# Kernel tuning notes

Measured on AMD Instinct MI355X. Metric: run time of the kernel, lower is better.

## Reference

```python
import jax, jax.numpy as jnp
import numpy as np

N_NODES = 50000
N_EDGES = 800000
IN_FEATS, N_HIDDEN, OUT_FEATS = 512, 512, 256


def setup_inputs() -> dict:
    key = jax.random.key(0)
    ks = jax.random.split(key, 10)
    features = jax.random.normal(ks[0], (N_NODES, IN_FEATS), dtype=jnp.float32)
    src = jax.random.randint(ks[1], (N_EDGES,), 0, N_NODES, dtype=jnp.int64)
    dst = jax.random.randint(ks[2], (N_EDGES,), 0, N_NODES, dtype=jnp.int64)
    def glorot(k, fan_in, fan_out):
        s = jnp.sqrt(6.0 / (fan_in + fan_out)).astype(jnp.float32)
        return jax.random.uniform(k, (fan_in, fan_out), jnp.float32, -s, s)
    W0 = glorot(ks[3], IN_FEATS, N_HIDDEN)
    b0 = jnp.zeros((N_HIDDEN,), jnp.float32)
    W1 = glorot(ks[4], N_HIDDEN, N_HIDDEN)
    b1 = jnp.zeros((N_HIDDEN,), jnp.float32)
    W2 = glorot(ks[5], N_HIDDEN, OUT_FEATS)
    b2 = jnp.zeros((OUT_FEATS,), jnp.float32)
    return {"features": features, "src": src, "dst": dst,
            "W0": W0, "b0": b0, "W1": W1, "b1": b1, "W2": W2, "b2": b2}


def _graph_conv(x, W, b, src, dst, out_norm, in_norm, activation):
    # DGL GraphConv, norm='both': D_out^{-1/2} A^T D_in^{-1/2}? -> per-node scale,
    # gather on src, segment-sum on dst, scale, linear, bias, activation.
    h = x @ W                               # [N, out] dense GEMM (weight applied first)
    h = h * out_norm[:, None]               # src-side degree norm
    msgs = h[src]                           # [E, out] gather
    agg = jax.ops.segment_sum(msgs, dst, num_segments=x.shape[0])  # [N, out]
    agg = agg * in_norm[:, None] + b
    return activation(agg) if activation is not None else agg


def reference(features, src, dst, W0, b0, W1, b1, W2, b2):
    n = features.shape[0]
    ones = jnp.ones((src.shape[0],), jnp.float32)
    out_deg = jnp.clip(jax.ops.segment_sum(ones, src, num_segments=n), 1.0)
    in_deg = jnp.clip(jax.ops.segment_sum(ones, dst, num_segments=n), 1.0)
    out_norm = jax.lax.rsqrt(out_deg)
    in_norm = jax.lax.rsqrt(in_deg)
    # eval mode: dropout between layers is identity
    h = _graph_conv(features, W0, b0, src, dst, out_norm, in_norm, jax.nn.relu)
    h = _graph_conv(h, W1, b1, src, dst, out_norm, in_norm, jax.nn.relu)
    h = _graph_conv(h, W2, b2, src, dst, out_norm, in_norm, None)
    return h
```

## Files before the change

### kernel.cpp

```cpp
#include <hip/hip_runtime.h>

#define N_NODES 50000
#define N_EDGES 800000

typedef __attribute__((ext_vector_type(8))) _Float16 half8;
typedef __attribute__((ext_vector_type(4))) float f32x4;
typedef __attribute__((ext_vector_type(8))) unsigned short ushort8;

static __device__ __forceinline__ unsigned short f2h(float f) {
    _Float16 h = (_Float16)f;
    return __builtin_bit_cast(unsigned short, h);
}
static __device__ __forceinline__ float h2f(unsigned short u) {
    return (float)__builtin_bit_cast(_Float16, u);
}

static __device__ __forceinline__ void async16(unsigned short* lds, const unsigned short* g) {
    __builtin_amdgcn_global_load_lds(
        (const __attribute__((address_space(1))) void*)g,
        (__attribute__((address_space(3))) void*)lds, 16, 0, 0);
}

__global__ void hist_kernel(const int* __restrict__ src, const int* __restrict__ dst,
                            int* __restrict__ outc, int* __restrict__ inc) {
    int i = blockIdx.x * blockDim.x + threadIdx.x;
    if (i < N_EDGES) {
        atomicAdd(&outc[src[i]], 1);
        atomicAdd(&inc[dst[i]], 1);
    }
}

__global__ void norm_kernel(const int* __restrict__ outc, const int* __restrict__ inc,
                            float* __restrict__ outn, float* __restrict__ inn) {
    int i = blockIdx.x * blockDim.x + threadIdx.x;
    if (i < N_NODES) {
        outn[i] = rsqrtf(fmaxf((float)outc[i], 1.0f));
        inn[i]  = rsqrtf(fmaxf((float)inc[i], 1.0f));
    }
}

__global__ __launch_bounds__(256) void scan1(const int* __restrict__ cnt,
                                             int* __restrict__ row_start,
                                             int* __restrict__ bsum, int n) {
    __shared__ int t[256];
    int tid = threadIdx.x;
    int i = blockIdx.x * 256 + tid;
    int v = (i < n) ? cnt[i] : 0;
    t[tid] = v;
    __syncthreads();
#pragma unroll
    for (int off = 1; off < 256; off <<= 1) {
        int x = (tid >= off) ? t[tid - off] : 0;
        __syncthreads();
        t[tid] += x;
        __syncthreads();
    }
    if (i < n) row_start[i] = t[tid] - v;
    if (tid == 255) bsum[blockIdx.x] = t[255];
}

__global__ __launch_bounds__(256) void scan2(int* __restrict__ bsum,
                                             int* __restrict__ boff,
                                             int* __restrict__ row_start, int nb) {
    __shared__ int t[256];
    int tid = threadIdx.x;
    int v = (tid < nb) ? bsum[tid] : 0;
    t[tid] = v;
    __syncthreads();
#pragma unroll
    for (int off = 1; off < 256; off <<= 1) {
        int x = (tid >= off) ? t[tid - off] : 0;
        __syncthreads();
        t[tid] += x;
        __syncthreads();
    }
    if (tid < nb) boff[tid] = t[tid] - v;
    if (tid == 0) row_start[N_NODES] = N_EDGES;
}

__global__ __launch_bounds__(256) void scan3(int* __restrict__ row_start,
                                             const int* __restrict__ boff, int n) {
    int i = blockIdx.x * 256 + threadIdx.x;
    if (i < n) row_start[i] += boff[blockIdx.x];
}

__global__ __launch_bounds__(256) void bucket_hist(const int* __restrict__ inc,
                                                   int* __restrict__ bcnt) {
    __shared__ int lh[1024];
    int tid = threadIdx.x;
    for (int b = tid; b < 1024; b += 256) lh[b] = 0;
    __syncthreads();
    int i = blockIdx.x * 256 + tid;
    if (i < N_NODES) atomicAdd(&lh[min(inc[i], 1023)], 1);
    __syncthreads();
    for (int b = tid; b < 1024; b += 256) {
        int v = lh[b];
        if (v) atomicAdd(&bcnt[b], v);
    }
}

__global__ __launch_bounds__(1024) void bucket_scan(const int* __restrict__ bcnt,
                                                    int* __restrict__ boff2) {
    __shared__ int t[1024];
    int tid = threadIdx.x;
    int v = bcnt[tid];
    t[tid] = v;
    __syncthreads();
#pragma unroll
    for (int off = 1; off < 1024; off <<= 1) {
        int x = (tid >= off) ? t[tid - off] : 0;
        __syncthreads();
        t[tid] += x;
        __syncthreads();
    }
    boff2[tid] = t[tid] - v;
}

__global__ __launch_bounds__(256) void bucket_scatter(const int* __restrict__ inc,
                               int* __restrict__ bcur,
                               int* __restrict__ porder, int* __restrict__ rank,
                               int* __restrict__ pdeg) {
    __shared__ int lcnt[1024];
    __shared__ int gbase[1024];
    int tid = threadIdx.x;
    for (int b = tid; b < 1024; b += 256) lcnt[b] = 0;
    __syncthreads();
    int i = blockIdx.x * 256 + tid;
    int deg = 0, bkt = 0, lpos = 0;
    if (i < N_NODES) {
        deg = inc[i];
        bkt = min(deg, 1023);
        lpos = atomicAdd(&lcnt[bkt], 1);
    }
    __syncthreads();
    for (int b = tid; b < 1024; b += 256) {
        int v = lcnt[b];
        if (v) gbase[b] = atomicAdd(&bcur[b], v);
    }
    __syncthreads();
    if (i < N_NODES) {
        int p = gbase[bkt] + lpos;
        porder[p] = i;
        rank[i] = p;
        pdeg[p] = deg;
    }
}

__global__ void fill_kernel(const int* __restrict__ src, const int* __restrict__ dst,
                            const int* __restrict__ rank, const int* __restrict__ prow,
                            int* __restrict__ cursor, int* __restrict__ csr2) {
    int e = blockIdx.x * blockDim.x + threadIdx.x;
    if (e < N_EDGES) {
        int d = dst[e];
        int pos = atomicAdd(&cursor[d], 1);
        csr2[prow[rank[d]] + pos] = src[e];
    }
}

__global__ __launch_bounds__(256) void conv_W(const float* __restrict__ W,
                                              unsigned short* __restrict__ Wt,
                                              int K, int N) {
    __shared__ float t[32][33];
    int tx = threadIdx.x & 31, ty = threadIdx.x >> 5;
    int kb = blockIdx.x * 32, nb = blockIdx.y * 32;
#pragma unroll
    for (int i = 0; i < 4; ++i)
        t[ty + 8 * i][tx] = W[(size_t)(kb + ty + 8 * i) * N + nb + tx];
    __syncthreads();
#pragma unroll
    for (int i = 0; i < 4; ++i) {
        float v = t[tx][ty + 8 * i];
        int n = nb + ty + 8 * i, k = kb + tx;
        Wt[(size_t)n * K + k] = f2h(v);
    }
}

__global__ void conv_A(const float4* __restrict__ feat4, const float* __restrict__ outn,
                       ushort4* __restrict__ Af, long total4) {
    long i = (long)blockIdx.x * blockDim.x + threadIdx.x;
    if (i >= total4) return;
    int row = (int)(i >> 7);
    float s = outn[row];
    float4 v = feat4[i];
    ushort4 h;
    h.x = f2h(v.x * s);
    h.y = f2h(v.y * s);
    h.z = f2h(v.z * s);
    h.w = f2h(v.w * s);
    Af[i] = h;
}

__global__ __launch_bounds__(256) void gemm_mfma(
    const unsigned short* __restrict__ A, const unsigned short* __restrict__ B,
    unsigned short* __restrict__ C, int M, int N)
{
    const int K = 512;
    __shared__ unsigned short sA[128 * 32];
    __shared__ unsigned short sB[128 * 32];

    const int tid = threadIdx.x;
    const int rowBase = blockIdx.x * 128;
    const int colBase = blockIdx.y * 128;
    const int wave = tid >> 6;
    const int lane = tid & 63;
    const int wr = (wave >> 1) * 64;
    const int wc = (wave & 1) * 64;
    const int lrow = lane & 15;
    const int quad = lane >> 4;

    f32x4 acc[4][4] = {};

    const int crow = tid >> 2;
    const int ck   = (tid & 3) * 8;
    const int ar0 = min(rowBase + crow, M - 1);
    const int ar1 = min(rowBase + 64 + crow, M - 1);
    const int bn0 = colBase + crow;
    const int bn1 = colBase + 64 + crow;
    const int ldsOf0 = tid * 8;
    const int ldsOf1 = 64 * 32 + tid * 8;

    for (int k0 = 0; k0 < K; k0 += 32) {
        __syncthreads();
        async16(sA + ldsOf0, A + (size_t)ar0 * K + k0 + ck);
        async16(sA + ldsOf1, A + (size_t)ar1 * K + k0 + ck);
        async16(sB + ldsOf0, B + (size_t)bn0 * K + k0 + ck);
        async16(sB + ldsOf1, B + (size_t)bn1 * K + k0 + ck);
        __syncthreads();

        half8 av[4], bv[4];
#pragma unroll
        for (int mt = 0; mt < 4; ++mt)
            av[mt] = *(const half8*)&sA[(wr + mt * 16 + lrow) * 32 + quad * 8];
#pragma unroll
        for (int nt = 0; nt < 4; ++nt)
            bv[nt] = *(const half8*)&sB[(wc + nt * 16 + lrow) * 32 + quad * 8];
#pragma unroll
        for (int mt = 0; mt < 4; ++mt)
#pragma unroll
            for (int nt = 0; nt < 4; ++nt)
                acc[mt][nt] = __builtin_amdgcn_mfma_f32_16x16x32_f16(av[mt], bv[nt], acc[mt][nt], 0, 0, 0);
    }

#pragma unroll
    for (int mt = 0; mt < 4; ++mt) {
        int grow0 = rowBase + wr + mt * 16 + quad * 4;
#pragma unroll
        for (int nt = 0; nt < 4; ++nt) {
            int gcol = colBase + wc + nt * 16 + lrow;
            size_t chunkBase = (size_t)(gcol >> 5) * M * 32 + (gcol & 31);
#pragma unroll
            for (int r = 0; r < 4; ++r) {
                int grow = grow0 + r;
                if (grow < M) C[chunkBase + (size_t)grow * 32] = f2h(acc[mt][nt][r]);
            }
        }
    }
}

#define SLAB 1024

#define GATHER8(ACC, HSRC, K0)                                                  \
    {                                                                           \
        int i0 = slab[(K0) + 0], i1 = slab[(K0) + 1];                           \
        int i2 = slab[(K0) + 2], i3 = slab[(K0) + 3];                           \
        int i4 = slab[(K0) + 4], i5 = slab[(K0) + 5];                           \
        int i6 = slab[(K0) + 6], i7 = slab[(K0) + 7];                           \
        const ushort8 u0 = *(const ushort8*)(HSRC + (unsigned)i0 * 32u + fo);   \
        const ushort8 u1 = *(const ushort8*)(HSRC + (unsigned)i1 * 32u + fo);   \
        const ushort8 u2 = *(const ushort8*)(HSRC + (unsigned)i2 * 32u + fo);   \
        const ushort8 u3 = *(const ushort8*)(HSRC + (unsigned)i3 * 32u + fo);   \
        const ushort8 u4 = *(const ushort8*)(HSRC + (unsigned)i4 * 32u + fo);   \
        const ushort8 u5 = *(const ushort8*)(HSRC + (unsigned)i5 * 32u + fo);   \
        const ushort8 u6 = *(const ushort8*)(HSRC + (unsigned)i6 * 32u + fo);   \
        const ushort8 u7 = *(const ushort8*)(HSRC + (unsigned)i7 * 32u + fo);   \
        _Pragma("unroll")                                                       \
        for (int q = 0; q < 8; ++q) {                                           \
            ACC[q] += h2f(u0[q]); ACC[q] += h2f(u1[q]);                         \
            ACC[q] += h2f(u2[q]); ACC[q] += h2f(u3[q]);                         \
            ACC[q] += h2f(u4[q]); ACC[q] += h2f(u5[q]);                         \
            ACC[q] += h2f(u6[q]); ACC[q] += h2f(u7[q]);                         \
        }                                                                       \
    }

#define GATHER1(ACC, HSRC, K0)                                                  \
    {                                                                           \
        int idx = slab[(K0)];                                                   \
        const ushort8 u = *(const ushort8*)(HSRC + (unsigned)idx * 32u + fo);   \
        _Pragma("unroll")                                                       \
        for (int q = 0; q < 8; ++q) ACC[q] += h2f(u[q]);                        \
    }

__global__ __launch_bounds__(256) void agg_f16_v8(
    const unsigned short* __restrict__ H, const int* __restrict__ csr2,
    const int* __restrict__ porder, const int* __restrict__ prow,
    const float* __restrict__ inn, const float* __restrict__ outn,
    const float* __restrict__ bias, unsigned short* __restrict__ Af)
{
    __shared__ int sIdx[4][SLAB];
    const int tid = threadIdx.x, lane = tid & 63, w = tid >> 6;
    const int s = lane >> 2, f = lane & 3;
    const unsigned fo = (unsigned)f * 8u;
    const int c = blockIdx.z * 8 + blockIdx.x;
    const int ty = (int)gridDim.y - 1 - (int)blockIdx.y;
    const int t = ty * 64 + w * 16 + s;

    int d = 0, st = N_EDGES, en = N_EDGES;
    if (t < N_NODES) {
        d  = porder[t];
        st = prow[t];
        en = prow[t + 1];
    }
    const int eStart = __shfl(st, 0);
    const int eEnd   = __shfl(en, 63);

    const unsigned short* Hc = H + (size_t)c * (N_NODES * 32);
    int* slab = sIdx[w];
    float a[8] = {};

    for (int b = eStart; b < eEnd; b += SLAB) {
        const int nstage = min(eEnd - b, SLAB);
        for (int i = lane; i < nstage; i += 64)
            slab[i] = __builtin_nontemporal_load(csr2 + b + i);
        asm volatile("s_waitcnt lgkmcnt(0)" ::: "memory");

        const int js = max(st, b);
        const int je = min(en, b + nstage);
        int k = js;
        for (; k + 8 <= je; k += 8) GATHER8(a, Hc, k - b);
        for (; k < je; ++k) GATHER1(a, Hc, k - b);
        asm volatile("" ::: "memory");
    }

    if (t < N_NODES) {
        float si = inn[d], so = outn[d];
        float b8[8];
        *(float4*)&b8[0] = *(const float4*)(bias + c * 32 + f * 8);
        *(float4*)&b8[4] = *(const float4*)(bias + c * 32 + f * 8 + 4);
        ushort8 h;
#pragma unroll
        for (int q = 0; q < 8; ++q)
            h[q] = f2h(fmaxf(a[q] * si + b8[q], 0.f) * so);
        __builtin_nontemporal_store(h,
            (ushort8*)(Af + (size_t)d * 512 + c * 32 + f * 8));
    }
}

__global__ __launch_bounds__(256) void agg_f32_v8(
    const unsigned short* __restrict__ H, const int* __restrict__ csr2,
    const int* __restrict__ porder, const int* __restrict__ prow,
    const float* __restrict__ inn, const float* __restrict__ bias,
    float* __restrict__ out)
{
    __shared__ int sIdx[4][SLAB];
    const int tid = threadIdx.x, lane = tid & 63, w = tid >> 6;
    const int s = lane >> 2, f = lane & 3;
    const unsigned fo = (unsigned)f * 8u;
    const int c = blockIdx.x;
    const int ty = (int)gridDim.y - 1 - (int)blockIdx.y;
    const int t = ty * 64 + w * 16 + s;

    int d = 0, st = N_EDGES, en = N_EDGES;
    if (t < N_NODES) {
        d  = porder[t];
        st = prow[t];
        en = prow[t + 1];
    }
    const int eStart = __shfl(st, 0);
    const int eEnd   = __shfl(en, 63);

    const unsigned short* Hc = H + (size_t)c * (N_NODES * 32);
    int* slab = sIdx[w];
    float a[8] = {};

    for (int b = eStart; b < eEnd; b += SLAB) {
        const int nstage = min(eEnd - b, SLAB);
        for (int i = lane; i < nstage; i += 64)
            slab[i] = __builtin_nontemporal_load(csr2 + b + i);
        asm volatile("s_waitcnt lgkmcnt(0)" ::: "memory");

        const int js = max(st, b);
        const int je = min(en, b + nstage);
        int k = js;
        for (; k + 8 <= je; k += 8) GATHER8(a, Hc, k - b);
        for (; k < je; ++k) GATHER1(a, Hc, k - b);
        asm volatile("" ::: "memory");
    }

    if (t < N_NODES) {
        float si = inn[d];
        float b8[8];
        *(float4*)&b8[0] = *(const float4*)(bias + c * 32 + f * 8);
        *(float4*)&b8[4] = *(const float4*)(bias + c * 32 + f * 8 + 4);
        f32x4 r0, r1;
        r0.x = a[0] * si + b8[0]; r0.y = a[1] * si + b8[1];
        r0.z = a[2] * si + b8[2]; r0.w = a[3] * si + b8[3];
        r1.x = a[4] * si + b8[4]; r1.y = a[5] * si + b8[5];
        r1.z = a[6] * si + b8[6]; r1.w = a[7] * si + b8[7];
        float* op = out + (size_t)d * 256 + c * 32 + f * 8;
        __builtin_nontemporal_store(r0, (f32x4*)op);
        __builtin_nontemporal_store(r1, (f32x4*)(op + 4));
    }
}

extern "C" void kernel_launch(void* const* d_in, const int* in_sizes, int n_in,
                              void* d_out, int out_size, void* d_ws, size_t ws_size,
                              hipStream_t stream) {
    const float* feat = (const float*)d_in[0];
    const int*   src  = (const int*)d_in[1];
    const int*   dst  = (const int*)d_in[2];
    const float* W0   = (const float*)d_in[3];
    const float* b0   = (const float*)d_in[4];
    const float* W1   = (const float*)d_in[5];
    const float* b1   = (const float*)d_in[6];
    const float* W2   = (const float*)d_in[7];
    const float* b2   = (const float*)d_in[8];
    float* out = (float*)d_out;

    char* p = (char*)d_ws;
    auto alloc = [&](size_t bytes) {
        char* r = p;
        p += (bytes + 63) & ~(size_t)63;
        return r;
    };
    float* outn = (float*)alloc(N_NODES * 4);
    float* inn  = (float*)alloc(N_NODES * 4);
    int* outc      = (int*)alloc(N_NODES * 4);
    int* inc       = (int*)alloc(N_NODES * 4);
    int* cursor    = (int*)alloc(N_NODES * 4);
    int* bcnt      = (int*)alloc(1024 * 4);
    int* porder    = (int*)alloc(N_NODES * 4);
    int* rank      = (int*)alloc(N_NODES * 4);
    int* pdeg      = (int*)alloc(N_NODES * 4);
    int* prow      = (int*)alloc((N_NODES + 1) * 4);
    int* bsum      = (int*)alloc(256 * 4);
    int* boff      = (int*)alloc(256 * 4);
    int* boff2     = (int*)alloc(1024 * 4);
    int* csr2      = (int*)alloc(N_EDGES * 4);
    unsigned short* W0t = (unsigned short*)alloc(512 * 512 * 2);
    unsigned short* W1t = (unsigned short*)alloc(512 * 512 * 2);
    unsigned short* W2t = (unsigned short*)alloc(256 * 512 * 2);
    unsigned short* Af  = (unsigned short*)alloc((size_t)N_NODES * 512 * 2);
    unsigned short* H   = (unsigned short*)alloc((size_t)N_NODES * 512 * 2);

    const int NB = (N_NODES + 255) / 256;

    hipMemsetAsync(outc, 0, (size_t)3 * N_NODES * 4 + 1024 * 4, stream);
    hist_kernel<<<(N_EDGES + 255) / 256, 256, 0, stream>>>(src, dst, outc, inc);
    norm_kernel<<<(N_NODES + 255) / 256, 256, 0, stream>>>(outc, inc, outn, inn);
    bucket_hist<<<NB, 256, 0, stream>>>(inc, bcnt);
    bucket_scan<<<1, 1024, 0, stream>>>(bcnt, boff2);
    bucket_scatter<<<NB, 256, 0, stream>>>(inc, boff2, porder, rank, pdeg);
    scan1<<<NB, 256, 0, stream>>>(pdeg, prow, bsum, N_NODES);
    scan2<<<1, 256, 0, stream>>>(bsum, boff, prow, NB);
    scan3<<<NB, 256, 0, stream>>>(prow, boff, N_NODES);
    fill_kernel<<<(N_EDGES + 255) / 256, 256, 0, stream>>>(src, dst, rank, prow, cursor, csr2);

    conv_W<<<dim3(16, 16), 256, 0, stream>>>(W0, W0t, 512, 512);
    conv_W<<<dim3(16, 16), 256, 0, stream>>>(W1, W1t, 512, 512);
    conv_W<<<dim3(16, 8),  256, 0, stream>>>(W2, W2t, 512, 256);

    long total4 = (long)N_NODES * 128;
    conv_A<<<(int)((total4 + 255) / 256), 256, 0, stream>>>(
        (const float4*)feat, outn, (ushort4*)Af, total4);

    dim3 g512((N_NODES + 127) / 128, 4);
    dim3 g256((N_NODES + 127) / 128, 2);
    const int NTB = (N_NODES + 63) / 64;
    dim3 gAgg512(8, NTB, 2);
    dim3 gAgg256(8, NTB);

    gemm_mfma<<<g512, 256, 0, stream>>>(Af, W0t, H, N_NODES, 512);
    agg_f16_v8<<<gAgg512, 256, 0, stream>>>(
        H, csr2, porder, prow, inn, outn, b0, Af);

    gemm_mfma<<<g512, 256, 0, stream>>>(Af, W1t, H, N_NODES, 512);
    agg_f16_v8<<<gAgg512, 256, 0, stream>>>(
        H, csr2, porder, prow, inn, outn, b1, Af);

    gemm_mfma<<<g256, 256, 0, stream>>>(Af, W2t, H, N_NODES, 256);
    agg_f32_v8<<<gAgg256, 256, 0, stream>>>(
        H, csr2, porder, prow, inn, b2, out);
}
```

Baseline: 729.1 us.

## Make aggregation kernels persistent and fuse norm into bucket histogram

After: 755.2 us. +3.6%, slower.

```diff
diff --git a/kernel.cpp b/kernel.cpp
--- a/kernel.cpp
+++ b/kernel.cpp
@@ -2,6 +2,8 @@
 
 #define N_NODES 50000
 #define N_EDGES 800000
+#define NTB ((N_NODES + 63) / 64)
+#define NPB 256
 
 typedef __attribute__((ext_vector_type(8))) _Float16 half8;
 typedef __attribute__((ext_vector_type(4))) float f32x4;
@@ -27,15 +29,6 @@
     if (i < N_EDGES) {
         atomicAdd(&outc[src[i]], 1);
         atomicAdd(&inc[dst[i]], 1);
-    }
-}
-
-__global__ void norm_kernel(const int* __restrict__ outc, const int* __restrict__ inc,
-                            float* __restrict__ outn, float* __restrict__ inn) {
-    int i = blockIdx.x * blockDim.x + threadIdx.x;
-    if (i < N_NODES) {
-        outn[i] = rsqrtf(fmaxf((float)outc[i], 1.0f));
-        inn[i]  = rsqrtf(fmaxf((float)inc[i], 1.0f));
     }
 }
 
@@ -84,14 +77,20 @@
     if (i < n) row_start[i] += boff[blockIdx.x];
 }
 
-__global__ __launch_bounds__(256) void bucket_hist(const int* __restrict__ inc,
-                                                   int* __restrict__ bcnt) {
+__global__ __launch_bounds__(256) void bucket_hist_norm(
+        const int* __restrict__ inc, const int* __restrict__ outc,
+        int* __restrict__ bcnt, float* __restrict__ outn, float* __restrict__ inn) {
     __shared__ int lh[1024];
     int tid = threadIdx.x;
     for (int b = tid; b < 1024; b += 256) lh[b] = 0;
     __syncthreads();
     int i = blockIdx.x * 256 + tid;
-    if (i < N_NODES) atomicAdd(&lh[min(inc[i], 1023)], 1);
+    if (i < N_NODES) {
+        int dc = inc[i];
+        atomicAdd(&lh[min(dc, 1023)], 1);
+        outn[i] = rsqrtf(fmaxf((float)outc[i], 1.0f));
+        inn[i]  = rsqrtf(fmaxf((float)dc, 1.0f));
+    }
     __syncthreads();
     for (int b = tid; b < 1024; b += 256) {
         int v = lh[b];
@@ -118,8 +117,7 @@
 
 __global__ __launch_bounds__(256) void bucket_scatter(const int* __restrict__ inc,
                                int* __restrict__ bcur,
-                               int* __restrict__ porder, int* __restrict__ rank,
-                               int* __restrict__ pdeg) {
+                               int* __restrict__ porder, int* __restrict__ pdeg) {
     __shared__ int lcnt[1024];
     __shared__ int gbase[1024];
     int tid = threadIdx.x;
@@ -141,19 +139,24 @@
     if (i < N_NODES) {
         int p = gbase[bkt] + lpos;
         porder[p] = i;
-        rank[i] = p;
         pdeg[p] = deg;
     }
 }
 
+__global__ void write_base2(const int* __restrict__ porder, const int* __restrict__ prow,
+                            int* __restrict__ base2) {
+    int p = blockIdx.x * blockDim.x + threadIdx.x;
+    if (p < N_NODES) base2[porder[p]] = prow[p];
+}
+
 __global__ void fill_kernel(const int* __restrict__ src, const int* __restrict__ dst,
-                            const int* __restrict__ rank, const int* __restrict__ prow,
+                            const int* __restrict__ base2,
                             int* __restrict__ cursor, int* __restrict__ csr2) {
     int e = blockIdx.x * blockDim.x + threadIdx.x;
     if (e < N_EDGES) {
         int d = dst[e];
         int pos = atomicAdd(&cursor[d], 1);
-        csr2[prow[rank[d]] + pos] = src[e];
+        csr2[base2[d] + pos] = src[e];
     }
 }
 
@@ -290,7 +293,7 @@
         for (int q = 0; q < 8; ++q) ACC[q] += h2f(u[q]);                        \
     }
 
-__global__ __launch_bounds__(256) void agg_f16_v8(
+__global__ __launch_bounds__(256) void agg_f16_v9(
     const unsigned short* __restrict__ H, const int* __restrict__ csr2,
     const int* __restrict__ porder, const int* __restrict__ prow,
     const float* __restrict__ inn, const float* __restrict__ outn,
@@ -300,52 +303,61 @@
     const int tid = threadIdx.x, lane = tid & 63, w = tid >> 6;
     const int s = lane >> 2, f = lane & 3;
     const unsigned fo = (unsigned)f * 8u;
-    const int c = blockIdx.z * 8 + blockIdx.x;
-    const int ty = (int)gridDim.y - 1 - (int)blockIdx.y;
-    const int t = ty * 64 + w * 16 + s;
-
-    int d = 0, st = N_EDGES, en = N_EDGES;
-    if (t < N_NODES) {
-        d  = porder[t];
-        st = prow[t];
-        en = prow[t + 1];
-    }
-    const int eStart = __shfl(st, 0);
-    const int eEnd   = __shfl(en, 63);
-
-    const unsigned short* Hc = H + (size_t)c * (N_NODES * 32);
+    const int x = blockIdx.x;
     int* slab = sIdx[w];
-    float a[8] = {};
-
-    for (int b = eStart; b < eEnd; b += SLAB) {
-        const int nstage = min(eEnd - b, SLAB);
-        for (int i = lane; i < nstage; i += 64)
-            slab[i] = __builtin_nontemporal_load(csr2 + b + i);
-        asm volatile("s_waitcnt lgkmcnt(0)" ::: "memory");
-
-        const int js = max(st, b);
-        const int je = min(en, b + nstage);
-        int k = js;
-        for (; k + 8 <= je; k += 8) GATHER8(a, Hc, k - b);
-        for (; k < je; ++k) GATHER1(a, Hc, k - b);
-        asm volatile("" ::: "memory");
-    }
-
-    if (t < N_NODES) {
-        float si = inn[d], so = outn[d];
-        float b8[8];
-        *(float4*)&b8[0] = *(const float4*)(bias + c * 32 + f * 8);
-        *(float4*)&b8[4] = *(const float4*)(bias + c * 32 + f * 8 + 4);
-        ushort8 h;
-#pragma unroll
-        for (int q = 0; q < 8; ++q)
-            h[q] = f2h(fmaxf(a[q] * si + b8[q], 0.f) * so);
-        __builtin_nontemporal_store(h,
-            (ushort8*)(Af + (size_t)d * 512 + c * 32 + f * 8));
-    }
-}
-
-__global__ __launch_bounds__(256) void agg_f32_v8(
+
+    for (int phase = 0; phase < 2; ++phase) {
+        const int c = phase * 8 + x;
+        const unsigned short* Hc = H + (size_t)c * (N_NODES * 32);
+        const float4 bq0 = *(const float4*)(bias + c * 32 + f * 8);
+        const float4 bq1 = *(const float4*)(bias + c * 32 + f * 8 + 4);
+
+        for (int j = blockIdx.y; j < NTB; j += NPB) {
+            const int ty = NTB - 1 - j;
+            const int t = ty * 64 + w * 16 + s;
+            int d = 0, st = N_EDGES, en = N_EDGES;
+            if (t < N_NODES) {
+                d  = porder[t];
+                st = prow[t];
+                en = prow[t + 1];
+            }
+            const int eStart = __shfl(st, 0);
+            const int eEnd   = __shfl(en, 63);
+
+            float a[8] = {};
+            for (int b = eStart; b < eEnd; b += SLAB) {
+                const int nstage = min(eEnd - b, SLAB);
+                for (int i = lane; i < nstage; i += 64)
+                    slab[i] = __builtin_nontemporal_load(csr2 + b + i);
+                asm volatile("s_waitcnt lgkmcnt(0)" ::: "memory");
+
+                const int js = max(st, b);
+                const int je = min(en, b + nstage);
+                int k = js;
+                for (; k + 8 <= je; k += 8) GATHER8(a, Hc, k - b);
+                for (; k < je; ++k) GATHER1(a, Hc, k - b);
+                asm volatile("" ::: "memory");
+            }
+
+            if (t < N_NODES) {
+                float si = inn[d], so = outn[d];
+                ushort8 h;
+                h[0] = f2h(fmaxf(a[0] * si + bq0.x, 0.f) * so);
+                h[1] = f2h(fmaxf(a[1] * si + bq0.y, 0.f) * so);
+                h[2] = f2h(fmaxf(a[2] * si + bq0.z, 0.f) * so);
+                h[3] = f2h(fmaxf(a[3] * si + bq0.w, 0.f) * so);
+                h[4] = f2h(fmaxf(a[4] * si + bq1.x, 0.f) * so);
+                h[5] = f2h(fmaxf(a[5] * si + bq1.y, 0.f) * so);
+                h[6] = f2h(fmaxf(a[6] * si + bq1.z, 0.f) * so);
+                h[7] = f2h(fmaxf(a[7] * si + bq1.w, 0.f) * so);
+                __builtin_nontemporal_store(h,
+                    (ushort8*)(Af + (size_t)d * 512 + c * 32 + f * 8));
+            }
+        }
+    }
+}
+
+__global__ __launch_bounds__(256) void agg_f32_v9(
     const unsigned short* __restrict__ H, const int* __restrict__ csr2,
     const int* __restrict__ porder, const int* __restrict__ prow,
     const float* __restrict__ inn, const float* __restrict__ bias,
@@ -356,49 +368,50 @@
     const int s = lane >> 2, f = lane & 3;
     const unsigned fo = (unsigned)f * 8u;
     const int c = blockIdx.x;
-    const int ty = (int)gridDim.y - 1 - (int)blockIdx.y;
-    const int t = ty * 64 + w * 16 + s;
-
-    int d = 0, st = N_EDGES, en = N_EDGES;
-    if (t < N_NODES) {
-        d  = porder[t];
-        st = prow[t];
-        en = prow[t + 1];
-    }
-    const int eStart = __shfl(st, 0);
-    const int eEnd   = __shfl(en, 63);
+    int* slab = sIdx[w];
 
     const unsigned short* Hc = H + (size_t)c * (N_NODES * 32);
-    int* slab = sIdx[w];
-    float a[8] = {};
-
-    for (int b = eStart; b < eEnd; b += SLAB) {
-        const int nstage = min(eEnd - b, SLAB);
-        for (int i = lane; i < nstage; i += 64)
-            slab[i] = __builtin_nontemporal_load(csr2 + b + i);
-        asm volatile("s_waitcnt lgkmcnt(0)" ::: "memory");
-
-        const int js = max(st, b);
-        const int je = min(en, b + nstage);
-        int k = js;
-        for (; k + 8 <= je; k += 8) GATHER8(a, Hc, k - b);
-        for (; k < je; ++k) GATHER1(a, Hc, k - b);
-        asm volatile("" ::: "memory");
-    }
-
-    if (t < N_NODES) {
-        float si = inn[d];
-        float b8[8];
-        *(float4*)&b8[0] = *(const float4*)(bias + c * 32 + f * 8);
-        *(float4*)&b8[4] = *(const float4*)(bias + c * 32 + f * 8 + 4);
-        f32x4 r0, r1;
-        r0.x = a[0] * si + b8[0]; r0.y = a[1] * si + b8[1];
-        r0.z = a[2] * si + b8[2]; r0.w = a[3] * si + b8[3];
-        r1.x = a[4] * si + b8[4]; r1.y = a[5] * si + b8[5];
-        r1.z = a[6] * si + b8[6]; r1.w = a[7] * si + b8[7];
-        float* op = out + (size_t)d * 256 + c * 32 + f * 8;
-        __builtin_nontemporal_store(r0, (f32x4*)op);
-        __builtin_nontemporal_store(r1, (f32x4*)(op + 4));
+    const float4 bq0 = *(const float4*)(bias + c * 32 + f * 8);
+    const float4 bq1 = *(const float4*)(bias + c * 32 + f * 8 + 4);
+
+    for (int j = blockIdx.y; j < NTB; j += NPB) {
+        const int ty = NTB - 1 - j;
+        const int t = ty * 64 + w * 16 + s;
+        int d = 0, st = N_EDGES, en = N_EDGES;
+        if (t < N_NODES) {
+            d  = porder[t];
+            st = prow[t];
+            en = prow[t + 1];
+        }
+        const int eStart = __shfl(st, 0);
+        const int eEnd   = __shfl(en, 63);
+
+        float a[8] = {};
+        for (int b = eStart; b < eEnd; b += SLAB) {
+            const int nstage = min(eEnd - b, SLAB);
+            for (int i = lane; i < nstage; i += 64)
+                slab[i] = __builtin_nontemporal_load(csr2 + b + i);
+            asm volatile("s_waitcnt lgkmcnt(0)" ::: "memory");
+
+            const int js = max(st, b);
+            const int je = min(en, b + nstage);
+            int k = js;
+            for (; k + 8 <= je; k += 8) GATHER8(a, Hc, k - b);
+            for (; k < je; ++k) GATHER1(a, Hc, k - b);
+            asm volatile("" ::: "memory");
+        }
+
+        if (t < N_NODES) {
+            float si = inn[d];
+            f32x4 r0, r1;
+            r0.x = a[0] * si + bq0.x; r0.y = a[1] * si + bq0.y;
+            r0.z = a[2] * si + bq0.z; r0.w = a[3] * si + bq0.w;
+            r1.x = a[4] * si + bq1.x; r1.y = a[5] * si + bq1.y;
+            r1.z = a[6] * si + bq1.z; r1.w = a[7] * si + bq1.w;
+            float* op = out + (size_t)d * 256 + c * 32 + f * 8;
+            __builtin_nontemporal_store(r0, (f32x4*)op);
+            __builtin_nontemporal_store(r1, (f32x4*)(op + 4));
+        }
     }
 }
 
@@ -429,8 +442,8 @@
     int* cursor    = (int*)alloc(N_NODES * 4);
     int* bcnt      = (int*)alloc(1024 * 4);
     int* porder    = (int*)alloc(N_NODES * 4);
-    int* rank      = (int*)alloc(N_NODES * 4);
     int* pdeg      = (int*)alloc(N_NODES * 4);
+    int* base2     = (int*)alloc(N_NODES * 4);
     int* prow      = (int*)alloc((N_NODES + 1) * 4);
     int* bsum      = (int*)alloc(256 * 4);
     int* boff      = (int*)alloc(256 * 4);
@@ -446,14 +459,14 @@
 
     hipMemsetAsync(outc, 0, (size_t)3 * N_NODES * 4 + 1024 * 4, stream);
     hist_kernel<<<(N_EDGES + 255) / 256, 256, 0, stream>>>(src, dst, outc, inc);
-    norm_kernel<<<(N_NODES + 255) / 256, 256, 0, stream>>>(outc, inc, outn, inn);
-    bucket_hist<<<NB, 256, 0, stream>>>(inc, bcnt);
+    bucket_hist_norm<<<NB, 256, 0, stream>>>(inc, outc, bcnt, outn, inn);
     bucket_scan<<<1, 1024, 0, stream>>>(bcnt, boff2);
-    bucket_scatter<<<NB, 256, 0, stream>>>(inc, boff2, porder, rank, pdeg);
+    bucket_scatter<<<NB, 256, 0, stream>>>(inc, boff2, porder, pdeg);
     scan1<<<NB, 256, 0, stream>>>(pdeg, prow, bsum, N_NODES);
     scan2<<<1, 256, 0, stream>>>(bsum, boff, prow, NB);
     scan3<<<NB, 256, 0, stream>>>(prow, boff, N_NODES);
-    fill_kernel<<<(N_EDGES + 255) / 256, 256, 0, stream>>>(src, dst, rank, prow, cursor, csr2);
+    write_base2<<<NB, 256, 0, stream>>>(porder, prow, base2);
+    fill_kernel<<<(N_EDGES + 255) / 256, 256, 0, stream>>>(src, dst, base2, cursor, csr2);
 
     conv_W<<<dim3(16, 16), 256, 0, stream>>>(W0, W0t, 512, 512);
     conv_W<<<dim3(16, 16), 256, 0, stream>>>(W1, W1t, 512, 512);
@@ -465,19 +478,17 @@
 
     dim3 g512((N_NODES + 127) / 128, 4);
     dim3 g256((N_NODES + 127) / 128, 2);
-    const int NTB = (N_NODES + 63) / 64;
-    dim3 gAgg512(8, NTB, 2);
-    dim3 gAgg256(8, NTB);
+    dim3 gAgg(8, NPB);
 
     gemm_mfma<<<g512, 256, 0, stream>>>(Af, W0t, H, N_NODES, 512);
-    agg_f16_v8<<<gAgg512, 256, 0, stream>>>(
+    agg_f16_v9<<<gAgg, 256, 0, stream>>>(
         H, csr2, porder, prow, inn, outn, b0, Af);
 
     gemm_mfma<<<g512, 256, 0, stream>>>(Af, W1t, H, N_NODES, 512);
-    agg_f16_v8<<<gAgg512, 256, 0, stream>>>(
+    agg_f16_v9<<<gAgg, 256, 0, stream>>>(
         H, csr2, porder, prow, inn, outn, b1, Af);
 
     gemm_mfma<<<g256, 256, 0, stream>>>(Af, W2t, H, N_NODES, 256);
-    agg_f32_v8<<<gAgg256, 256, 0, stream>>>(
+    agg_f32_v9<<<gAgg, 256, 0, stream>>>(
         H, csr2, porder, prow, inn, b2, out);
 }
```

## Fuse CSR preprocessing kernels and derive row offsets from degree-bucket scan

Applied to the files above, without the earlier changes.

After: 718.3 us. No clear change (-1.5%).

```diff
diff --git a/kernel.cpp b/kernel.cpp
--- a/kernel.cpp
+++ b/kernel.cpp
@@ -2,6 +2,7 @@
 
 #define N_NODES 50000
 #define N_EDGES 800000
+#define NTB ((N_NODES + 63) / 64)
 
 typedef __attribute__((ext_vector_type(8))) _Float16 half8;
 typedef __attribute__((ext_vector_type(4))) float f32x4;
@@ -30,68 +31,20 @@
     }
 }
 
-__global__ void norm_kernel(const int* __restrict__ outc, const int* __restrict__ inc,
-                            float* __restrict__ outn, float* __restrict__ inn) {
-    int i = blockIdx.x * blockDim.x + threadIdx.x;
-    if (i < N_NODES) {
-        outn[i] = rsqrtf(fmaxf((float)outc[i], 1.0f));
-        inn[i]  = rsqrtf(fmaxf((float)inc[i], 1.0f));
-    }
-}
-
-__global__ __launch_bounds__(256) void scan1(const int* __restrict__ cnt,
-                                             int* __restrict__ row_start,
-                                             int* __restrict__ bsum, int n) {
-    __shared__ int t[256];
-    int tid = threadIdx.x;
-    int i = blockIdx.x * 256 + tid;
-    int v = (i < n) ? cnt[i] : 0;
-    t[tid] = v;
-    __syncthreads();
-#pragma unroll
-    for (int off = 1; off < 256; off <<= 1) {
-        int x = (tid >= off) ? t[tid - off] : 0;
-        __syncthreads();
-        t[tid] += x;
-        __syncthreads();
-    }
-    if (i < n) row_start[i] = t[tid] - v;
-    if (tid == 255) bsum[blockIdx.x] = t[255];
-}
-
-__global__ __launch_bounds__(256) void scan2(int* __restrict__ bsum,
-                                             int* __restrict__ boff,
-                                             int* __restrict__ row_start, int nb) {
-    __shared__ int t[256];
-    int tid = threadIdx.x;
-    int v = (tid < nb) ? bsum[tid] : 0;
-    t[tid] = v;
-    __syncthreads();
-#pragma unroll
-    for (int off = 1; off < 256; off <<= 1) {
-        int x = (tid >= off) ? t[tid - off] : 0;
-        __syncthreads();
-        t[tid] += x;
-        __syncthreads();
-    }
-    if (tid < nb) boff[tid] = t[tid] - v;
-    if (tid == 0) row_start[N_NODES] = N_EDGES;
-}
-
-__global__ __launch_bounds__(256) void scan3(int* __restrict__ row_start,
-                                             const int* __restrict__ boff, int n) {
-    int i = blockIdx.x * 256 + threadIdx.x;
-    if (i < n) row_start[i] += boff[blockIdx.x];
-}
-
-__global__ __launch_bounds__(256) void bucket_hist(const int* __restrict__ inc,
-                                                   int* __restrict__ bcnt) {
+__global__ __launch_bounds__(256) void bucket_hist_norm(
+        const int* __restrict__ inc, const int* __restrict__ outc,
+        int* __restrict__ bcnt, float* __restrict__ outn, float* __restrict__ inn) {
     __shared__ int lh[1024];
     int tid = threadIdx.x;
     for (int b = tid; b < 1024; b += 256) lh[b] = 0;
     __syncthreads();
     int i = blockIdx.x * 256 + tid;
-    if (i < N_NODES) atomicAdd(&lh[min(inc[i], 1023)], 1);
+    if (i < N_NODES) {
+        int dc = inc[i];
+        atomicAdd(&lh[min(dc, 1023)], 1);
+        outn[i] = rsqrtf(fmaxf((float)outc[i], 1.0f));
+        inn[i]  = rsqrtf(fmaxf((float)dc, 1.0f));
+    }
     __syncthreads();
     for (int b = tid; b < 1024; b += 256) {
         int v = lh[b];
@@ -100,26 +53,38 @@
 }
 
 __global__ __launch_bounds__(1024) void bucket_scan(const int* __restrict__ bcnt,
-                                                    int* __restrict__ boff2) {
+                                                    int* __restrict__ bcur,
+                                                    int* __restrict__ n0,
+                                                    int* __restrict__ e0,
+                                                    int* __restrict__ prow) {
     __shared__ int t[1024];
+    __shared__ int u[1024];
     int tid = threadIdx.x;
     int v = bcnt[tid];
+    int w = v * tid;
     t[tid] = v;
+    u[tid] = w;
     __syncthreads();
 #pragma unroll
     for (int off = 1; off < 1024; off <<= 1) {
         int x = (tid >= off) ? t[tid - off] : 0;
+        int y = (tid >= off) ? u[tid - off] : 0;
         __syncthreads();
         t[tid] += x;
+        u[tid] += y;
         __syncthreads();
     }
-    boff2[tid] = t[tid] - v;
+    bcur[tid] = t[tid] - v;
+    n0[tid]   = t[tid] - v;
+    e0[tid]   = u[tid] - w;
+    if (tid == 0) prow[N_NODES] = N_EDGES;
 }
 
 __global__ __launch_bounds__(256) void bucket_scatter(const int* __restrict__ inc,
                                int* __restrict__ bcur,
-                               int* __restrict__ porder, int* __restrict__ rank,
-                               int* __restrict__ pdeg) {
+                               const int* __restrict__ n0, const int* __restrict__ e0,
+                               int* __restrict__ porder, int* __restrict__ prow,
+                               int* __restrict__ base2) {
     __shared__ int lcnt[1024];
     __shared__ int gbase[1024];
     int tid = threadIdx.x;
@@ -140,29 +105,38 @@
     __syncthreads();
     if (i < N_NODES) {
         int p = gbase[bkt] + lpos;
+        int rs = e0[bkt] + (p - n0[bkt]) * deg;
         porder[p] = i;
-        rank[i] = p;
-        pdeg[p] = deg;
+        prow[p] = rs;
+        base2[i] = rs;
     }
 }
 
 __global__ void fill_kernel(const int* __restrict__ src, const int* __restrict__ dst,
-                            const int* __restrict__ rank, const int* __restrict__ prow,
+                            const int* __restrict__ base2,
                             int* __restrict__ cursor, int* __restrict__ csr2) {
     int e = blockIdx.x * blockDim.x + threadIdx.x;
     if (e < N_EDGES) {
         int d = dst[e];
         int pos = atomicAdd(&cursor[d], 1);
-        csr2[prow[rank[d]] + pos] = src[e];
-    }
-}
-
-__global__ __launch_bounds__(256) void conv_W(const float* __restrict__ W,
-                                              unsigned short* __restrict__ Wt,
-                                              int K, int N) {
+        csr2[base2[d] + pos] = src[e];
+    }
+}
+
+__global__ __launch_bounds__(256) void conv_W3(
+        const float* __restrict__ W0, const float* __restrict__ W1,
+        const float* __restrict__ W2, unsigned short* __restrict__ Wt0,
+        unsigned short* __restrict__ Wt1, unsigned short* __restrict__ Wt2) {
+    const int l = blockIdx.z;
+    const float* W = (l == 0) ? W0 : (l == 1) ? W1 : W2;
+    unsigned short* Wt = (l == 0) ? Wt0 : (l == 1) ? Wt1 : Wt2;
+    const int K = 512;
+    const int N = (l == 2) ? 256 : 512;
+    int nb = blockIdx.y * 32;
+    if (nb >= N) return;
     __shared__ float t[32][33];
     int tx = threadIdx.x & 31, ty = threadIdx.x >> 5;
-    int kb = blockIdx.x * 32, nb = blockIdx.y * 32;
+    int kb = blockIdx.x * 32;
 #pragma unroll
     for (int i = 0; i < 4; ++i)
         t[ty + 8 * i][tx] = W[(size_t)(kb + ty + 8 * i) * N + nb + tx];
@@ -429,12 +403,11 @@
     int* cursor    = (int*)alloc(N_NODES * 4);
     int* bcnt      = (int*)alloc(1024 * 4);
     int* porder    = (int*)alloc(N_NODES * 4);
-    int* rank      = (int*)alloc(N_NODES * 4);
-    int* pdeg      = (int*)alloc(N_NODES * 4);
+    int* base2     = (int*)alloc(N_NODES * 4);
     int* prow      = (int*)alloc((N_NODES + 1) * 4);
-    int* bsum      = (int*)alloc(256 * 4);
-    int* boff      = (int*)alloc(256 * 4);
-    int* boff2     = (int*)alloc(1024 * 4);
+    int* bcur      = (int*)alloc(1024 * 4);
+    int* n0        = (int*)alloc(1024 * 4);
+    int* e0        = (int*)alloc(1024 * 4);
     int* csr2      = (int*)alloc(N_EDGES * 4);
     unsigned short* W0t = (unsigned short*)alloc(512 * 512 * 2);
     unsigned short* W1t = (unsigned short*)alloc(512 * 512 * 2);
@@ -446,18 +419,12 @@
 
     hipMemsetAsync(outc, 0, (size_t)3 * N_NODES * 4 + 1024 * 4, stream);
     hist_kernel<<<(N_EDGES + 255) / 256, 256, 0, stream>>>(src, dst, outc, inc);
-    norm_kernel<<<(N_NODES + 255) / 256, 256, 0, stream>>>(outc, inc, outn, inn);
-    bucket_hist<<<NB, 256, 0, stream>>>(inc, bcnt);
-    bucket_scan<<<1, 1024, 0, stream>>>(bcnt, boff2);
-    bucket_scatter<<<NB, 256, 0, stream>>>(inc, boff2, porder, rank, pdeg);
-    scan1<<<NB, 256, 0, stream>>>(pdeg, prow, bsum, N_NODES);
-    scan2<<<1, 256, 0, stream>>>(bsum, boff, prow, NB);
-    scan3<<<NB, 256, 0, stream>>>(prow, boff, N_NODES);
-    fill_kernel<<<(N_EDGES + 255) / 256, 256, 0, stream>>>(src, dst, rank, prow, cursor, csr2);
-
-    conv_W<<<dim3(16, 16), 256, 0, stream>>>(W0, W0t, 512, 512);
-    conv_W<<<dim3(16, 16), 256, 0, stream>>>(W1, W1t, 512, 512);
-    conv_W<<<dim3(16, 8),  256, 0, stream>>>(W2, W2t, 512, 256);
+    bucket_hist_norm<<<NB, 256, 0, stream>>>(inc, outc, bcnt, outn, inn);
+    bucket_scan<<<1, 1024, 0, stream>>>(bcnt, bcur, n0, e0, prow);
+    bucket_scatter<<<NB, 256, 0, stream>>>(inc, bcur, n0, e0, porder, prow, base2);
+    fill_kernel<<<(N_EDGES + 255) / 256, 256, 0, stream>>>(src, dst, base2, cursor, csr2);
+
+    conv_W3<<<dim3(16, 16, 3), 256, 0, stream>>>(W0, W1, W2, W0t, W1t, W2t);
 
     long total4 = (long)N_NODES * 128;
     conv_A<<<(int)((total4 + 255) / 256), 256, 0, stream>>>(
@@ -465,7 +432,6 @@
 
     dim3 g512((N_NODES + 127) / 128, 4);
     dim3 g256((N_NODES + 127) / 128, 2);
-    const int NTB = (N_NODES + 63) / 64;
     dim3 gAgg512(8, NTB, 2);
     dim3 gAgg256(8, NTB);
 
```
